# Performance work log

Measured on AMD Instinct MI355X. Metric: run time of the kernel, lower is better.

Reference implementation:

```python
import jax, jax.numpy as jnp
import numpy as np

B, R, C = 4, 36, 3          # batch, n_rotations, kernel_dim/output_dim
H, W = 384, 224             # padded image spatial: (320+64, 160+64)
CROP = 64
PAD = CROP // 2             # pad_size = 32


def setup_inputs() -> dict:
    key = jax.random.key(0)
    k1, k2 = jax.random.split(key)
    logits = jax.random.normal(k1, (B, C, H, W), dtype=jnp.float32)
    kernel = jax.random.normal(k2, (B * R, C, CROP, CROP), dtype=jnp.float32)
    return {"logits": logits, "kernel": kernel}


def _correlate(logits, kernel):
    # Original computes a full B x (B*R) cross-correlation via F.conv2d and then
    # discards all off-diagonal blocks. A grouped conv (feature_group_count=B)
    # computes exactly the kept diagonal blocks: group i correlates sample i's
    # feature map with that sample's R rotated kernels. interpolate/crop are
    # per-channel/per-pixel so they commute with the channel selection -> same math.
    b, c, h, w = logits.shape
    r = kernel.shape[0] // b
    x = logits.reshape(1, b * c, h, w)
    out = jax.lax.conv_general_dilated(
        x, kernel,
        window_strides=(1, 1),
        padding=[(PAD, PAD), (PAD, PAD)],
        dimension_numbers=("NCHW", "OIHW", "NCHW"),
        feature_group_count=b,
    )  # [1, b*r, h+1, w+1]  (h + 2*PAD - CROP + 1 = h + 1)
    out = out.reshape(b, r, out.shape[-2], out.shape[-1])
    # F.interpolate(..., mode='bilinear', align_corners=False) == half-pixel
    # bilinear resize without antialiasing.
    out = jax.image.resize(out, (b, r, h, w), method="bilinear", antialias=False)
    out = out[:, :, PAD:-PAD, PAD:-PAD]  # [b, r, h-2*PAD, w-2*PAD] = [b, r, 320, 160]
    hc, wc = out.shape[-2], out.shape[-1]
    # softmax over the flattened per-sample (rotation x spatial) map
    flat = jax.nn.softmax(out.reshape(b, -1), axis=-1)
    return flat.reshape(b, r, hc, wc)


def reference(logits, kernel):
    return _correlate(logits, kernel)
```

## Files before the change

### kernel.cpp

```cpp
#include <hip/hip_runtime.h>

typedef short bf16x8 __attribute__((ext_vector_type(8)));
typedef float f32x4  __attribute__((ext_vector_type(4)));
typedef unsigned short u16;

#define B_ 4
#define R_ 36
#define RP 48
#define C_ 3
#define H_ 384
#define W_ 224
#define KS 64
#define OY 321
#define OX 161
#define HC 320
#define WC 160
#define LCOLS 128
#define PITCH 120
#define GR 3072
#define BLKS_PER_BATCH 7200

__device__ __forceinline__ u16 bf16rtn(float v) {
    union { float f; unsigned u; } U; U.f = v;
    unsigned r = U.u + 0x7fffu + ((U.u >> 16) & 1u);
    return (u16)(r >> 16);
}
__device__ __forceinline__ float bf16tof(u16 h) {
    union { float f; unsigned u; } U; U.u = ((unsigned)h) << 16; return U.f;
}

__device__ __forceinline__ float wave_max(float v) {
    #pragma unroll
    for (int off = 32; off > 0; off >>= 1) v = fmaxf(v, __shfl_down(v, off, 64));
    return v;
}
__device__ __forceinline__ float wave_sum(float v) {
    #pragma unroll
    for (int off = 32; off > 0; off >>= 1) v += __shfl_down(v, off, 64);
    return v;
}

__global__ __launch_bounds__(256) void prep_weights(
    const float* __restrict__ wk, u16* __restrict__ wa)
{
    int d = blockIdx.x * 256 + threadIdx.x;
    int ky32  = d & 31;
    int t1    = d >> 5;
    int r     = t1 % 48;
    int t2    = t1 / 48;
    int plane = t2 & 1;
    int g2    = t2 >> 1;
    int kycp  = g2 & 1;
    int kx    = (g2 >> 1) & 63;
    int bc    = g2 >> 7;
    int c     = bc % 3;
    int b     = bc / 3;
    int ky    = kycp*32 + ky32;
    float v = 0.f;
    if (r < R_) v = wk[(((size_t)(b*R_ + r)*C_ + c)*KS + ky)*KS + kx];
    u16 h = bf16rtn(v);
    u16 o = plane ? bf16rtn(v - bf16tof(h)) : h;
    wa[(size_t)g2*GR + plane*1536 + r*32 + (ky32 ^ (((r >> 1) & 3) << 3))] = o;
}

template<int NT>
__device__ __forceinline__ void conv_body(
    const float* __restrict__ in, const u16* __restrict__ wa,
    float* __restrict__ out, u16* Lh, u16* Ll, int x0, int y0)
{
    const int b    = blockIdx.z;
    const int t    = threadIdx.x;
    const int w    = __builtin_amdgcn_readfirstlane(t >> 6);
    const int lane = t & 63;
    const int nu   = lane & 15;
    const int q    = lane >> 4;

    f32x4 acc[3][NT];
    #pragma unroll
    for (int mi = 0; mi < 3; mi++)
        #pragma unroll
        for (int n = 0; n < NT; n++)
            acc[mi][n] = (f32x4){0.f, 0.f, 0.f, 0.f};

    const u16* gbase = wa + (size_t)(b*384)*GR;

    const int sw   = (8*q) ^ (((nu >> 1) & 3) << 3);
    const int offH = nu*32 + sw;

    bf16x8 A0h[3], A0l[3], A1h[3], A1l[3];

    #pragma unroll
    for (int mi = 0; mi < 3; mi++) {
        A0h[mi] = *(const bf16x8*)(gbase + offH + mi*512);
        A0l[mi] = *(const bf16x8*)(gbase + 1536 + offH + mi*512);
    }

#define STEP(G, CH, CL, NH, NL) do {                                         \
    int gn_ = (G) + 1; if (gn_ > 383) gn_ = 383;                             \
    const u16* gp_ = gbase + (size_t)gn_ * GR;                               \
    _Pragma("unroll")                                                        \
    for (int mi = 0; mi < 3; mi++) {                                         \
        NH[mi] = *(const bf16x8*)(gp_ + offH + mi*512);                      \
        NL[mi] = *(const bf16x8*)(gp_ + 1536 + offH + mi*512);               \
    }                                                                        \
    const int kx_   = ((G) & 127) >> 1;                                      \
    const int kycp_ = (G) & 1;                                               \
    const u16* cb_ = Lh + (size_t)(nu + kx_)*PITCH + 32*kycp_ + 8*q + 8*w;   \
    _Pragma("unroll")                                                        \
    for (int n0 = 0; n0 < NT; n0 += 2) {                                     \
        const u16* p0_ = cb_ + n0*16*PITCH;                                  \
        bf16x8 Bh0_ = *(const bf16x8*)p0_;                                   \
        bf16x8 Bl0_ = *(const bf16x8*)(p0_ + (size_t)LCOLS*PITCH);           \
        bf16x8 Bh1_ = Bh0_, Bl1_ = Bl0_;                                     \
        if (n0 + 1 < NT) {                                                   \
            const u16* p1_ = cb_ + (n0+1)*16*PITCH;                          \
            Bh1_ = *(const bf16x8*)p1_;                                      \
            Bl1_ = *(const bf16x8*)(p1_ + (size_t)LCOLS*PITCH);              \
        }                                                                    \
        __builtin_amdgcn_s_setprio(1);                                       \
        _Pragma("unroll")                                                    \
        for (int mi = 0; mi < 3; mi++)                                       \
            acc[mi][n0] = __builtin_amdgcn_mfma_f32_16x16x32_bf16(CH[mi], Bh0_, acc[mi][n0], 0, 0, 0); \
        if (n0 + 1 < NT) {                                                   \
            _Pragma("unroll")                                                \
            for (int mi = 0; mi < 3; mi++)                                   \
                acc[mi][n0+1] = __builtin_amdgcn_mfma_f32_16x16x32_bf16(CH[mi], Bh1_, acc[mi][n0+1], 0, 0, 0); \
        }                                                                    \
        _Pragma("unroll")                                                    \
        for (int mi = 0; mi < 3; mi++)                                       \
            acc[mi][n0] = __builtin_amdgcn_mfma_f32_16x16x32_bf16(CH[mi], Bl0_, acc[mi][n0], 0, 0, 0); \
        if (n0 + 1 < NT) {                                                   \
            _Pragma("unroll")                                                \
            for (int mi = 0; mi < 3; mi++)                                   \
                acc[mi][n0+1] = __builtin_amdgcn_mfma_f32_16x16x32_bf16(CH[mi], Bl1_, acc[mi][n0+1], 0, 0, 0); \
        }                                                                    \
        _Pragma("unroll")                                                    \
        for (int mi = 0; mi < 3; mi++)                                       \
            acc[mi][n0] = __builtin_amdgcn_mfma_f32_16x16x32_bf16(CL[mi], Bh0_, acc[mi][n0], 0, 0, 0); \
        if (n0 + 1 < NT) {                                                   \
            _Pragma("unroll")                                                \
            for (int mi = 0; mi < 3; mi++)                                   \
                acc[mi][n0+1] = __builtin_amdgcn_mfma_f32_16x16x32_bf16(CL[mi], Bh1_, acc[mi][n0+1], 0, 0, 0); \
        }                                                                    \
        __builtin_amdgcn_s_setprio(0);                                       \
    }                                                                        \
} while (0)

    for (int c = 0; c < C_; c++) {
        __syncthreads();
        const float* src = in + ((size_t)(b*C_ + c))*H_*W_;
        #pragma unroll
        for (int k = 0; k < 4; k++) {
            int idx = t + 512*k;
            if (idx < 1920) {
                int a    = idx & 31;
                int pr   = (idx >> 5) + ((a >> 3) & 3);
                if (pr >= 60) pr -= 60;
                int r0   = pr * 2;
                int c4   = a * 4;
                int gx   = x0 + c4;
                int gy   = y0 + r0;
                float4 va = make_float4(0.f,0.f,0.f,0.f), vb = va;
                if (gx < W_) {
                    if (gy < H_)     va = *(const float4*)(src + (size_t)gy*W_ + gx);
                    if (gy + 1 < H_) vb = *(const float4*)(src + (size_t)(gy+1)*W_ + gx);
                }
                const float* pa = &va.x;
                const float* pb = &vb.x;
                #pragma unroll
                for (int j = 0; j < 4; j++) {
                    int col = c4 + j;
                    u16 ha = bf16rtn(pa[j]);
                    u16 hb = bf16rtn(pb[j]);
                    u16 la = bf16rtn(pa[j] - bf16tof(ha));
                    u16 lb = bf16rtn(pb[j] - bf16tof(hb));
                    *(unsigned*)&Lh[col*PITCH + r0] = (unsigned)ha | ((unsigned)hb << 16);
                    *(unsigned*)&Ll[col*PITCH + r0] = (unsigned)la | ((unsigned)lb << 16);
                }
            }
        }
        __syncthreads();

        #pragma unroll 1
        for (int gi2 = 0; gi2 < 128; gi2 += 2) {
            const int g = c*128 + gi2;
            STEP(g,     A0h, A0l, A1h, A1l);
            STEP(g + 1, A1h, A1l, A0h, A0l);
        }
    }
#undef STEP

    {
        const int y = y0 + 8*w;
        if (y <= 320) {
            #pragma unroll
            for (int mi = 0; mi < 3; mi++) {
                #pragma unroll
                for (int n = 0; n < NT; n++) {
                    #pragma unroll
                    for (int i = 0; i < 4; i++) {
                        int r = mi*16 + q*4 + i;
                        int x = x0 + n*16 + nu;
                        if (r < R_ && x < OX)
                            out[((size_t)(b*R_ + r)*OY + y)*OX + x] = acc[mi][n][i];
                    }
                }
            }
        }
    }
}

__global__ __launch_bounds__(512, 4) void conv_mfma(
    const float* __restrict__ in, const u16* __restrict__ wa, float* __restrict__ out)
{
    __shared__ __align__(16) u16 smem[2*LCOLS*PITCH];
    u16* Lh = smem;
    u16* Ll = smem + LCOLS*PITCH;
    const int s  = blockIdx.y;
    const int y0 = (s < 40) ? ((s >> 3)*64 + (s & 7)) : 320;

    if (blockIdx.x == 0)      conv_body<4>(in, wa, out, Lh, Ll, 0,   y0);
    else if (blockIdx.x == 1) conv_body<4>(in, wa, out, Lh, Ll, 64,  y0);
    else                      conv_body<3>(in, wa, out, Lh, Ll, 128, y0);
}

__global__ __launch_bounds__(256) void resize_kernel(
    const float* __restrict__ cv, float* __restrict__ out, float* __restrict__ pmax)
{
    const int t = threadIdx.x;
    const int idx = blockIdx.x * 256 + t;
    const int j = idx % WC;
    const int rest = idx / WC;
    const int i = rest % HC;
    const int br = rest / HC;

    float fy = (i + 32.5f) * (1.0f/384.0f);
    float fx = (j + 32.5f) * (1.0f/224.0f);

    const float* p = cv + ((size_t)br*OY + i)*OX + j;
    float v00 = p[0], v01 = p[1], v10 = p[OX], v11 = p[OX+1];
    float v = (1.f-fy)*((1.f-fx)*v00 + fx*v01) + fy*((1.f-fx)*v10 + fx*v11);
    out[idx] = v;

    __shared__ float sm[4];
    float m = wave_max(v);
    if ((t & 63) == 0) sm[t >> 6] = m;
    __syncthreads();
    if (t == 0) pmax[blockIdx.x] = fmaxf(fmaxf(sm[0], sm[1]), fmaxf(sm[2], sm[3]));
}

__global__ __launch_bounds__(256) void reduce_kernel(
    const float* __restrict__ part, float* __restrict__ res, int n, int is_sum)
{
    const int b = blockIdx.x;
    const int t = threadIdx.x;
    const float* p = part + (size_t)b*n;
    float v = is_sum ? 0.f : -3.0e38f;
    for (int k = t; k < n; k += 256) v = is_sum ? (v + p[k]) : fmaxf(v, p[k]);
    __shared__ float sm[4];
    float w = is_sum ? wave_sum(v) : wave_max(v);
    if ((t & 63) == 0) sm[t >> 6] = w;
    __syncthreads();
    if (t == 0) {
        res[b] = is_sum ? (sm[0]+sm[1]+sm[2]+sm[3])
                        : fmaxf(fmaxf(sm[0], sm[1]), fmaxf(sm[2], sm[3]));
    }
}

__global__ __launch_bounds__(256) void exp_kernel(
    float* __restrict__ out, const float* __restrict__ bmax, float* __restrict__ psum)
{
    const int t = threadIdx.x;
    const int idx = blockIdx.x * 256 + t;
    const int b = blockIdx.x / BLKS_PER_BATCH;
    float e = expf(out[idx] - bmax[b]);
    out[idx] = e;
    __shared__ float sm[4];
    float s = wave_sum(e);
    if ((t & 63) == 0) sm[t >> 6] = s;
    __syncthreads();
    if (t == 0) psum[blockIdx.x] = sm[0]+sm[1]+sm[2]+sm[3];
}

__global__ __launch_bounds__(256) void scale_kernel(
    float* __restrict__ out, const float* __restrict__ bsum)
{
    const int idx = blockIdx.x * 256 + threadIdx.x;
    const int b = blockIdx.x / BLKS_PER_BATCH;
    out[idx] = out[idx] / bsum[b];
}

extern "C" void kernel_launch(void* const* d_in, const int* in_sizes, int n_in,
                              void* d_out, int out_size, void* d_ws, size_t ws_size,
                              hipStream_t stream)
{
    const float* logits = (const float*)d_in[0];
    const float* wk     = (const float*)d_in[1];
    float* out = (float*)d_out;
    char*  wsB = (char*)d_ws;

    float* convOut = (float*)wsB;
    u16*   wa      = (u16*)(wsB + 29768256);
    float* pmax    = (float*)(wsB + 29768256 + 9437184);
    float* psum    = pmax + 28800;
    float* bmax    = psum + 28800;
    float* bsum    = bmax + 8;

    hipLaunchKernelGGL(prep_weights, dim3(18432), dim3(256), 0, stream, wk, wa);
    hipLaunchKernelGGL(conv_mfma,    dim3(3, 41, B_), dim3(512), 0, stream, logits, wa, convOut);
    hipLaunchKernelGGL(resize_kernel, dim3(28800), dim3(256), 0, stream, convOut, out, pmax);
    hipLaunchKernelGGL(reduce_kernel, dim3(4),     dim3(256), 0, stream, pmax, bmax, BLKS_PER_BATCH, 0);
    hipLaunchKernelGGL(exp_kernel,    dim3(28800), dim3(256), 0, stream, out, bmax, psum);
    hipLaunchKernelGGL(reduce_kernel, dim3(4),     dim3(256), 0, stream, psum, bsum, BLKS_PER_BATCH, 1);
    hipLaunchKernelGGL(scale_kernel,  dim3(28800), dim3(256), 0, stream, out, bsum);
}
```

Measured before the change: 673.3 us.

## Replace reduction kernels with atomics, remap conv grid, batch MFMA B-loads

```diff
diff --git a/kernel.cpp b/kernel.cpp
--- a/kernel.cpp
+++ b/kernel.cpp
@@ -29,6 +29,15 @@
     union { float f; unsigned u; } U; U.u = ((unsigned)h) << 16; return U.f;
 }
 
+__device__ __forceinline__ unsigned fenc(float f) {
+    unsigned u = __float_as_uint(f);
+    return u ^ ((u >> 31) ? 0xFFFFFFFFu : 0x80000000u);
+}
+__device__ __forceinline__ float fdec(unsigned e) {
+    unsigned u = e ^ ((e & 0x80000000u) ? 0x80000000u : 0xFFFFFFFFu);
+    return __uint_as_float(u);
+}
+
 __device__ __forceinline__ float wave_max(float v) {
     #pragma unroll
     for (int off = 32; off > 0; off >>= 1) v = fmaxf(v, __shfl_down(v, off, 64));
@@ -41,9 +50,11 @@
 }
 
 __global__ __launch_bounds__(256) void prep_weights(
-    const float* __restrict__ wk, u16* __restrict__ wa)
+    const float* __restrict__ wk, u16* __restrict__ wa,
+    unsigned* __restrict__ umax, float* __restrict__ bsum)
 {
     int d = blockIdx.x * 256 + threadIdx.x;
+    if (d < 8) { umax[d] = 0u; bsum[d] = 0.f; }
     int ky32  = d & 31;
     int t1    = d >> 5;
     int r     = t1 % 48;
@@ -66,9 +77,8 @@
 template<int NT>
 __device__ __forceinline__ void conv_body(
     const float* __restrict__ in, const u16* __restrict__ wa,
-    float* __restrict__ out, u16* Lh, u16* Ll, int x0, int y0)
-{
-    const int b    = blockIdx.z;
+    float* __restrict__ out, u16* Lh, u16* Ll, int x0, int y0, int b)
+{
     const int t    = threadIdx.x;
     const int w    = __builtin_amdgcn_readfirstlane(t >> 6);
     const int lane = t & 63;
@@ -106,44 +116,30 @@
     const int kx_   = ((G) & 127) >> 1;                                      \
     const int kycp_ = (G) & 1;                                               \
     const u16* cb_ = Lh + (size_t)(nu + kx_)*PITCH + 32*kycp_ + 8*q + 8*w;   \
-    _Pragma("unroll")                                                        \
-    for (int n0 = 0; n0 < NT; n0 += 2) {                                     \
-        const u16* p0_ = cb_ + n0*16*PITCH;                                  \
-        bf16x8 Bh0_ = *(const bf16x8*)p0_;                                   \
-        bf16x8 Bl0_ = *(const bf16x8*)(p0_ + (size_t)LCOLS*PITCH);           \
-        bf16x8 Bh1_ = Bh0_, Bl1_ = Bl0_;                                     \
-        if (n0 + 1 < NT) {                                                   \
-            const u16* p1_ = cb_ + (n0+1)*16*PITCH;                          \
-            Bh1_ = *(const bf16x8*)p1_;                                      \
-            Bl1_ = *(const bf16x8*)(p1_ + (size_t)LCOLS*PITCH);              \
-        }                                                                    \
-        __builtin_amdgcn_s_setprio(1);                                       \
+    bf16x8 Bh_[NT], Bl_[NT];                                                 \
+    _Pragma("unroll")                                                        \
+    for (int n = 0; n < NT; n++) {                                           \
+        const u16* pn_ = cb_ + n*16*PITCH;                                   \
+        Bh_[n] = *(const bf16x8*)pn_;                                        \
+        Bl_[n] = *(const bf16x8*)(pn_ + (size_t)LCOLS*PITCH);                \
+    }                                                                        \
+    __builtin_amdgcn_s_setprio(1);                                           \
+    _Pragma("unroll")                                                        \
+    for (int n = 0; n < NT; n++)                                             \
         _Pragma("unroll")                                                    \
         for (int mi = 0; mi < 3; mi++)                                       \
-            acc[mi][n0] = __builtin_amdgcn_mfma_f32_16x16x32_bf16(CH[mi], Bh0_, acc[mi][n0], 0, 0, 0); \
-        if (n0 + 1 < NT) {                                                   \
-            _Pragma("unroll")                                                \
-            for (int mi = 0; mi < 3; mi++)                                   \
-                acc[mi][n0+1] = __builtin_amdgcn_mfma_f32_16x16x32_bf16(CH[mi], Bh1_, acc[mi][n0+1], 0, 0, 0); \
-        }                                                                    \
+            acc[mi][n] = __builtin_amdgcn_mfma_f32_16x16x32_bf16(CH[mi], Bh_[n], acc[mi][n], 0, 0, 0); \
+    _Pragma("unroll")                                                        \
+    for (int n = 0; n < NT; n++)                                             \
         _Pragma("unroll")                                                    \
         for (int mi = 0; mi < 3; mi++)                                       \
-            acc[mi][n0] = __builtin_amdgcn_mfma_f32_16x16x32_bf16(CH[mi], Bl0_, acc[mi][n0], 0, 0, 0); \
-        if (n0 + 1 < NT) {                                                   \
-            _Pragma("unroll")                                                \
-            for (int mi = 0; mi < 3; mi++)                                   \
-                acc[mi][n0+1] = __builtin_amdgcn_mfma_f32_16x16x32_bf16(CH[mi], Bl1_, acc[mi][n0+1], 0, 0, 0); \
-        }                                                                    \
+            acc[mi][n] = __builtin_amdgcn_mfma_f32_16x16x32_bf16(CH[mi], Bl_[n], acc[mi][n], 0, 0, 0); \
+    _Pragma("unroll")                                                        \
+    for (int n = 0; n < NT; n++)                                             \
         _Pragma("unroll")                                                    \
         for (int mi = 0; mi < 3; mi++)                                       \
-            acc[mi][n0] = __builtin_amdgcn_mfma_f32_16x16x32_bf16(CL[mi], Bh0_, acc[mi][n0], 0, 0, 0); \
-        if (n0 + 1 < NT) {                                                   \
-            _Pragma("unroll")                                                \
-            for (int mi = 0; mi < 3; mi++)                                   \
-                acc[mi][n0+1] = __builtin_amdgcn_mfma_f32_16x16x32_bf16(CL[mi], Bh1_, acc[mi][n0+1], 0, 0, 0); \
-        }                                                                    \
-        __builtin_amdgcn_s_setprio(0);                                       \
-    }                                                                        \
+            acc[mi][n] = __builtin_amdgcn_mfma_f32_16x16x32_bf16(CL[mi], Bh_[n], acc[mi][n], 0, 0, 0); \
+    __builtin_amdgcn_s_setprio(0);                                           \
 } while (0)
 
     for (int c = 0; c < C_; c++) {
@@ -216,16 +212,22 @@
     __shared__ __align__(16) u16 smem[2*LCOLS*PITCH];
     u16* Lh = smem;
     u16* Ll = smem + LCOLS*PITCH;
-    const int s  = blockIdx.y;
+
+    const int bx   = blockIdx.x;
+    const int b    = bx >> 1;
+    const int tile = 2*blockIdx.y + (bx & 1);
+    if (tile >= 123) return;
+    const int s    = tile / 3;
+    const int xsel = tile % 3;
     const int y0 = (s < 40) ? ((s >> 3)*64 + (s & 7)) : 320;
 
-    if (blockIdx.x == 0)      conv_body<4>(in, wa, out, Lh, Ll, 0,   y0);
-    else if (blockIdx.x == 1) conv_body<4>(in, wa, out, Lh, Ll, 64,  y0);
-    else                      conv_body<3>(in, wa, out, Lh, Ll, 128, y0);
+    if (xsel == 0)      conv_body<4>(in, wa, out, Lh, Ll, 0,   y0, b);
+    else if (xsel == 1) conv_body<4>(in, wa, out, Lh, Ll, 64,  y0, b);
+    else                conv_body<3>(in, wa, out, Lh, Ll, 128, y0, b);
 }
 
 __global__ __launch_bounds__(256) void resize_kernel(
-    const float* __restrict__ cv, float* __restrict__ out, float* __restrict__ pmax)
+    const float* __restrict__ cv, float* __restrict__ out, unsigned* __restrict__ umax)
 {
     const int t = threadIdx.x;
     const int idx = blockIdx.x * 256 + t;
@@ -246,40 +248,25 @@
     float m = wave_max(v);
     if ((t & 63) == 0) sm[t >> 6] = m;
     __syncthreads();
-    if (t == 0) pmax[blockIdx.x] = fmaxf(fmaxf(sm[0], sm[1]), fmaxf(sm[2], sm[3]));
-}
-
-__global__ __launch_bounds__(256) void reduce_kernel(
-    const float* __restrict__ part, float* __restrict__ res, int n, int is_sum)
-{
-    const int b = blockIdx.x;
-    const int t = threadIdx.x;
-    const float* p = part + (size_t)b*n;
-    float v = is_sum ? 0.f : -3.0e38f;
-    for (int k = t; k < n; k += 256) v = is_sum ? (v + p[k]) : fmaxf(v, p[k]);
-    __shared__ float sm[4];
-    float w = is_sum ? wave_sum(v) : wave_max(v);
-    if ((t & 63) == 0) sm[t >> 6] = w;
-    __syncthreads();
     if (t == 0) {
-        res[b] = is_sum ? (sm[0]+sm[1]+sm[2]+sm[3])
-                        : fmaxf(fmaxf(sm[0], sm[1]), fmaxf(sm[2], sm[3]));
+        float bm = fmaxf(fmaxf(sm[0], sm[1]), fmaxf(sm[2], sm[3]));
+        atomicMax(&umax[blockIdx.x / BLKS_PER_BATCH], fenc(bm));
     }
 }
 
 __global__ __launch_bounds__(256) void exp_kernel(
-    float* __restrict__ out, const float* __restrict__ bmax, float* __restrict__ psum)
+    float* __restrict__ out, const unsigned* __restrict__ umax, float* __restrict__ bsum)
 {
     const int t = threadIdx.x;
     const int idx = blockIdx.x * 256 + t;
     const int b = blockIdx.x / BLKS_PER_BATCH;
-    float e = expf(out[idx] - bmax[b]);
+    float e = expf(out[idx] - fdec(umax[b]));
     out[idx] = e;
     __shared__ float sm[4];
     float s = wave_sum(e);
     if ((t & 63) == 0) sm[t >> 6] = s;
     __syncthreads();
-    if (t == 0) psum[blockIdx.x] = sm[0]+sm[1]+sm[2]+sm[3];
+    if (t == 0) atomicAdd(&bsum[b], sm[0]+sm[1]+sm[2]+sm[3]);
 }
 
 __global__ __launch_bounds__(256) void scale_kernel(
@@ -299,18 +286,14 @@
     float* out = (float*)d_out;
     char*  wsB = (char*)d_ws;
 
-    float* convOut = (float*)wsB;
-    u16*   wa      = (u16*)(wsB + 29768256);
-    float* pmax    = (float*)(wsB + 29768256 + 9437184);
-    float* psum    = pmax + 28800;
-    float* bmax    = psum + 28800;
-    float* bsum    = bmax + 8;
-
-    hipLaunchKernelGGL(prep_weights, dim3(18432), dim3(256), 0, stream, wk, wa);
-    hipLaunchKernelGGL(conv_mfma,    dim3(3, 41, B_), dim3(512), 0, stream, logits, wa, convOut);
-    hipLaunchKernelGGL(resize_kernel, dim3(28800), dim3(256), 0, stream, convOut, out, pmax);
-    hipLaunchKernelGGL(reduce_kernel, dim3(4),     dim3(256), 0, stream, pmax, bmax, BLKS_PER_BATCH, 0);
-    hipLaunchKernelGGL(exp_kernel,    dim3(28800), dim3(256), 0, stream, out, bmax, psum);
-    hipLaunchKernelGGL(reduce_kernel, dim3(4),     dim3(256), 0, stream, psum, bsum, BLKS_PER_BATCH, 1);
+    float*    convOut = (float*)wsB;
+    u16*      wa      = (u16*)(wsB + 29768256);
+    unsigned* umax    = (unsigned*)(wsB + 29768256 + 9437184);
+    float*    bsum    = (float*)(wsB + 29768256 + 9437184 + 32);
+
+    hipLaunchKernelGGL(prep_weights, dim3(18432), dim3(256), 0, stream, wk, wa, umax, bsum);
+    hipLaunchKernelGGL(conv_mfma,    dim3(8, 62), dim3(512), 0, stream, logits, wa, convOut);
+    hipLaunchKernelGGL(resize_kernel, dim3(28800), dim3(256), 0, stream, convOut, out, umax);
+    hipLaunchKernelGGL(exp_kernel,    dim3(28800), dim3(256), 0, stream, out, umax, bsum);
     hipLaunchKernelGGL(scale_kernel,  dim3(28800), dim3(256), 0, stream, out, bsum);
 }
```

Result: slower. 1.593 ms (+136.5%).
